# Kernel tuning notes

Hardware: AMD Instinct MI355X
Metric: run time of the kernel (lower is better)

## Reference

```python
import jax, jax.numpy as jnp
import numpy as np

NUM_FIELDS = 40
EMBED_DIM = 64
ATTN_DIM = 32

def _triu_index(n):
    i, j = np.triu_indices(n, k=1)
    return jnp.asarray(i, jnp.int32), jnp.asarray(j, jnp.int32)

def setup_inputs() -> dict:
    key = jax.random.key(0)
    k0, k1, k2, k3, k4, k5 = jax.random.split(key, 6)
    B = 8192
    inputs = jax.random.normal(k0, (B, NUM_FIELDS, EMBED_DIM), dtype=jnp.float32)
    # attention MLP params (PyTorch Linear default init scale ~ 1/sqrt(fan_in))
    s1 = 1.0 / np.sqrt(EMBED_DIM)
    s2 = 1.0 / np.sqrt(ATTN_DIM)
    W1 = jax.random.uniform(k1, (EMBED_DIM, ATTN_DIM), jnp.float32, -s1, s1)
    b1 = jax.random.uniform(k2, (ATTN_DIM,), jnp.float32, -s1, s1)
    w2 = jax.random.uniform(k3, (ATTN_DIM,), jnp.float32, -s2, s2)
    p = jax.random.uniform(k4, (EMBED_DIM,), jnp.float32, -s1, s1)
    return {"inputs": inputs, "W1": W1, "b1": b1, "w2": w2, "p": p}

def reference(inputs, W1, b1, w2, p):
    idx0, idx1 = _triu_index(NUM_FIELDS)  # [P], P = 780 pairs
    # gather pairwise field embeddings and take elementwise product: [B, P, D]
    prod = inputs[:, idx0, :] * inputs[:, idx1, :]
    # tiny attention MLP: Linear -> ReLU -> Linear(no bias) -> softmax over pairs
    h = jax.nn.relu(jnp.einsum('bpd,da->bpa', prod, W1) + b1)  # [B, P, A]
    logits = jnp.einsum('bpa,a->bp', h, w2)                    # [B, P]
    attn = jax.nn.softmax(logits, axis=1)                      # softmax over pair dim
    # attention-weighted sum pooling over pairs: [B, D]
    pooled = jnp.einsum('bp,bpd->bd', attn, prod)
    # final linear projection to scalar (dropout=0 / eval -> identity)
    return jnp.einsum('bd,d->b', pooled, p)
```

## Files before the change

kernel.cpp:

```cpp
#include <hip/hip_runtime.h>


typedef _Float16 f16;
typedef f16 f16x2 __attribute__((ext_vector_type(2)));
typedef f16 f16x4 __attribute__((ext_vector_type(4)));
typedef f16 f16x8 __attribute__((ext_vector_type(8)));
typedef float fx16 __attribute__((ext_vector_type(16)));

#define NF 40
#define NB 8192
#define STR 76

union V8 { f16x8 v8; f16x4 v4[2]; f16x2 v2[4]; };

__global__ __launch_bounds__(256, 4) void afm_kernel(
    const float* __restrict__ x,
    const float* __restrict__ W1,
    const float* __restrict__ b1,
    const float* __restrict__ w2,
    const float* __restrict__ p,
    float* __restrict__ out)
{
    __shared__ f16 xh[4][NF * STR];

    const int wid  = threadIdx.x >> 6;
    const int lane = threadIdx.x & 63;
    const int b    = blockIdx.x * 4 + wid;
    f16* Xs = &xh[wid][0];

    const float4* xb = (const float4*)(x + (size_t)b * (NF * 64));
#pragma unroll
    for (int t = 0; t < 10; ++t) {
        int idx = t * 64 + lane;
        float4 v = xb[idx];
        f16x4 h = { (f16)v.x, (f16)v.y, (f16)v.z, (f16)v.w };
        int r = idx >> 4;
        int d = (idx & 15) * 4;
        *(f16x4*)(Xs + r * STR + d) = h;
    }
    __syncthreads();

    const int nl = lane & 31;
    const int hh = lane >> 5;
    const int h8 = hh * 8;

    V8 w1f[4];
#pragma unroll
    for (int kt = 0; kt < 4; ++kt)
#pragma unroll
        for (int j = 0; j < 8; ++j)
            w1f[kt].v8[j] = (f16)W1[(kt * 16 + h8 + j) * 32 + nl];

    f16x2 pp[16];
#pragma unroll
    for (int kt = 0; kt < 4; ++kt)
#pragma unroll
        for (int m = 0; m < 4; ++m) {
            f16x2 t2 = { (f16)p[kt * 16 + h8 + 2 * m], (f16)p[kt * 16 + h8 + 2 * m + 1] };
            pp[kt * 4 + m] = t2;
        }

    fx16 b1C;
    float w2v[16];
#pragma unroll
    for (int r = 0; r < 16; ++r) {
        int a = (r & 3) + 8 * (r >> 2) + 4 * hh;
        b1C[r] = b1[a];
        w2v[r] = w2[a];
    }

    f16x4 xif[8];
#pragma unroll
    for (int kt = 0; kt < 4; ++kt) {
        const f16* src = Xs + nl * STR + kt * 16 + h8;
        xif[2 * kt]     = *(const f16x4*)(src);
        xif[2 * kt + 1] = *(const f16x4*)(src + 4);
    }

    float accW = 0.f, accWS = 0.f;

    auto body = [&](const f16x4* xi, int jrow, bool valid) {
        const f16* base = Xs + jrow * STR + h8;
        V8 pr[4];
#pragma unroll
        for (int kt = 0; kt < 4; ++kt) {
            f16x4 a0 = *(const f16x4*)(base + kt * 16);
            f16x4 a1 = *(const f16x4*)(base + kt * 16 + 4);
            pr[kt].v4[0] = xi[2 * kt] * a0;
            pr[kt].v4[1] = xi[2 * kt + 1] * a1;
        }
        fx16 C = __builtin_amdgcn_mfma_f32_32x32x16_f16(w1f[0].v8, pr[0].v8, b1C, 0, 0, 0);
        C = __builtin_amdgcn_mfma_f32_32x32x16_f16(w1f[1].v8, pr[1].v8, C, 0, 0, 0);
        C = __builtin_amdgcn_mfma_f32_32x32x16_f16(w1f[2].v8, pr[2].v8, C, 0, 0, 0);
        C = __builtin_amdgcn_mfma_f32_32x32x16_f16(w1f[3].v8, pr[3].v8, C, 0, 0, 0);
        float sp = 0.f;
#pragma unroll
        for (int kt = 0; kt < 4; ++kt)
#pragma unroll
            for (int m = 0; m < 4; ++m)
                sp = __builtin_amdgcn_fdot2(pr[kt].v2[m], pp[kt * 4 + m], sp, false);
        float l0 = 0.f, l1 = 0.f;
#pragma unroll
        for (int r = 0; r < 8; ++r) {
            l0 = fmaf(fmaxf(C[2 * r], 0.f),     w2v[2 * r],     l0);
            l1 = fmaf(fmaxf(C[2 * r + 1], 0.f), w2v[2 * r + 1], l1);
        }
        float l = l0 + l1;
        l  += __shfl_xor(l, 32);
        sp += __shfl_xor(sp, 32);
        float w = valid ? __expf(l) : 0.f;
        accW += w;
        accWS = fmaf(w, sp, accWS);
    };

    for (int t = 1; t <= 16; ++t)
        body(xif, (nl + t) & 31, (t < 16) | (nl < 16));

    for (int u = 0; u < 8; ++u)
        body(xif, 32 + u, true);

    {
        int q = nl < 28 ? nl : 27;
        float disc = 225.0f - 8.0f * (float)q;
        int ii = (int)((15.0f - sqrtf(disc)) * 0.5f);
        if (ii * (15 - ii) / 2 > q) --ii;
        if ((ii + 1) * (14 - ii) / 2 <= q) ++ii;
        int jj = q - ii * (15 - ii) / 2 + ii + 1;
        int iC = 32 + ii, jC = 32 + jj;
        f16x4 xi2[8];
#pragma unroll
        for (int kt = 0; kt < 4; ++kt) {
            const f16* src = Xs + iC * STR + kt * 16 + h8;
            xi2[2 * kt]     = *(const f16x4*)(src);
            xi2[2 * kt + 1] = *(const f16x4*)(src + 4);
        }
        body(xi2, jC, nl < 28);
    }

#pragma unroll
    for (int m = 16; m >= 1; m >>= 1) {
        accW  += __shfl_xor(accW, m);
        accWS += __shfl_xor(accWS, m);
    }
    if (lane == 0) out[b] = accWS / accW;
}

extern "C" void kernel_launch(void* const* d_in, const int* in_sizes, int n_in,
                              void* d_out, int out_size, void* d_ws, size_t ws_size,
                              hipStream_t stream) {
    const float* x  = (const float*)d_in[0];
    const float* W1 = (const float*)d_in[1];
    const float* b1 = (const float*)d_in[2];
    const float* w2 = (const float*)d_in[3];
    const float* p  = (const float*)d_in[4];
    float* out = (float*)d_out;
    dim3 grid(NB / 4), block(256);
    hipLaunchKernelGGL(afm_kernel, grid, block, 0, stream, x, W1, b1, w2, p, out);
}
```

Measured before the change: 153.0 us.

## Compute p-projection with MFMA and pack ReLU/w2 logit dot into f16 fdot2

The p-projection of each pair product moves from 16 scalar fdot2 operations plus a cross-half shuffle to a second MFMA chain that reuses the same pr operands, with p broadcast as the A matrix. The logit reduction now packs ReLU'd accumulators to f16 pairs and uses fdot2 against w2 prescaled by log2(e), so the exponent becomes a native exp2. The peeled last iteration of the rotation loop removes the per-iteration validity predicate. The extra MFMA doubles matrix-core work per pair. The f16 rounding of hidden activations and logits lowers precision.

```diff
diff --git a/kernel.cpp b/kernel.cpp
--- a/kernel.cpp
+++ b/kernel.cpp
@@ -44,37 +44,44 @@
     const int hh = lane >> 5;
     const int h8 = hh * 8;
 
-    V8 w1f[4];
+    f16x8 w1f[4];
 #pragma unroll
     for (int kt = 0; kt < 4; ++kt)
 #pragma unroll
         for (int j = 0; j < 8; ++j)
-            w1f[kt].v8[j] = (f16)W1[(kt * 16 + h8 + j) * 32 + nl];
+            w1f[kt][j] = (f16)W1[(kt * 16 + h8 + j) * 32 + nl];
 
-    f16x2 pp[16];
+    f16x8 pA[4];
 #pragma unroll
     for (int kt = 0; kt < 4; ++kt)
 #pragma unroll
-        for (int m = 0; m < 4; ++m) {
-            f16x2 t2 = { (f16)p[kt * 16 + h8 + 2 * m], (f16)p[kt * 16 + h8 + 2 * m + 1] };
-            pp[kt * 4 + m] = t2;
-        }
+        for (int j = 0; j < 8; ++j)
+            pA[kt][j] = (f16)p[kt * 16 + h8 + j];
 
     fx16 b1C;
-    float w2v[16];
+    f16x2 w2h[8];
 #pragma unroll
     for (int r = 0; r < 16; ++r) {
         int a = (r & 3) + 8 * (r >> 2) + 4 * hh;
         b1C[r] = b1[a];
-        w2v[r] = w2[a];
     }
+#pragma unroll
+    for (int m = 0; m < 8; ++m) {
+        int r = 2 * m;
+        int a = (r & 3) + 8 * (r >> 2) + 4 * hh;
+        f16x2 t2 = { (f16)(w2[a] * 1.44269504f), (f16)(w2[a + 1] * 1.44269504f) };
+        w2h[m] = t2;
+    }
+    const float b1c0 = b1C[0];
 
     f16x4 xif[8];
+    {
+        const f16* src = Xs + nl * STR + h8;
 #pragma unroll
-    for (int kt = 0; kt < 4; ++kt) {
-        const f16* src = Xs + nl * STR + kt * 16 + h8;
-        xif[2 * kt]     = *(const f16x4*)(src);
-        xif[2 * kt + 1] = *(const f16x4*)(src + 4);
+        for (int kt = 0; kt < 4; ++kt) {
+            xif[2 * kt]     = *(const f16x4*)(src + kt * 16);
+            xif[2 * kt + 1] = *(const f16x4*)(src + kt * 16 + 4);
+        }
     }
 
     float accW = 0.f, accWS = 0.f;
@@ -89,32 +96,36 @@
             pr[kt].v4[0] = xi[2 * kt] * a0;
             pr[kt].v4[1] = xi[2 * kt + 1] * a1;
         }
-        fx16 C = __builtin_amdgcn_mfma_f32_32x32x16_f16(w1f[0].v8, pr[0].v8, b1C, 0, 0, 0);
-        C = __builtin_amdgcn_mfma_f32_32x32x16_f16(w1f[1].v8, pr[1].v8, C, 0, 0, 0);
-        C = __builtin_amdgcn_mfma_f32_32x32x16_f16(w1f[2].v8, pr[2].v8, C, 0, 0, 0);
-        C = __builtin_amdgcn_mfma_f32_32x32x16_f16(w1f[3].v8, pr[3].v8, C, 0, 0, 0);
-        float sp = 0.f;
-#pragma unroll
-        for (int kt = 0; kt < 4; ++kt)
-#pragma unroll
-            for (int m = 0; m < 4; ++m)
-                sp = __builtin_amdgcn_fdot2(pr[kt].v2[m], pp[kt * 4 + m], sp, false);
+        fx16 C  = __builtin_amdgcn_mfma_f32_32x32x16_f16(w1f[0], pr[0].v8, b1C, 0, 0, 0);
+        fx16 C2 = __builtin_amdgcn_mfma_f32_32x32x16_f16(pA[0],  pr[0].v8, b1C, 0, 0, 0);
+        C  = __builtin_amdgcn_mfma_f32_32x32x16_f16(w1f[1], pr[1].v8, C,  0, 0, 0);
+        C2 = __builtin_amdgcn_mfma_f32_32x32x16_f16(pA[1],  pr[1].v8, C2, 0, 0, 0);
+        C  = __builtin_amdgcn_mfma_f32_32x32x16_f16(w1f[2], pr[2].v8, C,  0, 0, 0);
+        C2 = __builtin_amdgcn_mfma_f32_32x32x16_f16(pA[2],  pr[2].v8, C2, 0, 0, 0);
+        C  = __builtin_amdgcn_mfma_f32_32x32x16_f16(w1f[3], pr[3].v8, C,  0, 0, 0);
+        C2 = __builtin_amdgcn_mfma_f32_32x32x16_f16(pA[3],  pr[3].v8, C2, 0, 0, 0);
+        float sp = C2[0] - b1c0;
+        const f16x2 z2 = { (f16)0.f, (f16)0.f };
         float l0 = 0.f, l1 = 0.f;
 #pragma unroll
-        for (int r = 0; r < 8; ++r) {
-            l0 = fmaf(fmaxf(C[2 * r], 0.f),     w2v[2 * r],     l0);
-            l1 = fmaf(fmaxf(C[2 * r + 1], 0.f), w2v[2 * r + 1], l1);
+        for (int m = 0; m < 8; ++m) {
+            f16x2 hm = __builtin_bit_cast(f16x2,
+                __builtin_amdgcn_cvt_pkrtz(C[2 * m], C[2 * m + 1]));
+            hm = __builtin_elementwise_max(hm, z2);
+            if (m & 1) l1 = __builtin_amdgcn_fdot2(hm, w2h[m], l1, false);
+            else       l0 = __builtin_amdgcn_fdot2(hm, w2h[m], l0, false);
         }
         float l = l0 + l1;
-        l  += __shfl_xor(l, 32);
-        sp += __shfl_xor(sp, 32);
-        float w = valid ? __expf(l) : 0.f;
+        l += __shfl_xor(l, 32);
+        float w = __builtin_amdgcn_exp2f(l);
+        if (!valid) w = 0.f;
         accW += w;
         accWS = fmaf(w, sp, accWS);
     };
 
-    for (int t = 1; t <= 16; ++t)
-        body(xif, (nl + t) & 31, (t < 16) | (nl < 16));
+    for (int t = 1; t <= 15; ++t)
+        body(xif, (nl + t) & 31, true);
+    body(xif, (nl + 16) & 31, nl < 16);
 
     for (int u = 0; u < 8; ++u)
         body(xif, 32 + u, true);
@@ -128,11 +139,11 @@
         int jj = q - ii * (15 - ii) / 2 + ii + 1;
         int iC = 32 + ii, jC = 32 + jj;
         f16x4 xi2[8];
+        const f16* src = Xs + iC * STR + h8;
 #pragma unroll
         for (int kt = 0; kt < 4; ++kt) {
-            const f16* src = Xs + iC * STR + kt * 16 + h8;
-            xi2[2 * kt]     = *(const f16x4*)(src);
-            xi2[2 * kt + 1] = *(const f16x4*)(src + 4);
+            xi2[2 * kt]     = *(const f16x4*)(src + kt * 16);
+            xi2[2 * kt + 1] = *(const f16x4*)(src + kt * 16 + 4);
         }
         body(xi2, jC, nl < 28);
     }
```

Measured after the change: 160.6 us. 5.0% more time.
